# Kernel optimization log

Measured on AMD Instinct MI355X. Metric: run time of the kernel, lower is better.

The kernel has to match this reference:

```python
import jax, jax.numpy as jnp
import numpy as np

N, E, D, K = 50000, 600000, 128, 8
EPS = 1e-09


def setup_inputs() -> dict:
    key = jax.random.key(0)
    ks = jax.random.split(key, 10)
    feature = jax.random.normal(ks[0], (N, D), dtype=jnp.float32)
    snorm_n = jax.random.uniform(ks[1], (N, 1), dtype=jnp.float32)
    src = jax.random.randint(ks[2], (E,), 0, N, dtype=jnp.int32)
    dst = jax.random.randint(ks[3], (E,), 0, N, dtype=jnp.int32)
    W_low = jax.random.normal(ks[4], (D, D), dtype=jnp.float32) / np.sqrt(D)
    W_high = jax.random.normal(ks[5], (D, D), dtype=jnp.float32) / np.sqrt(D)
    W_mid = jax.random.normal(ks[6], (D, D), dtype=jnp.float32) / np.sqrt(D)
    gamma_low = jax.random.uniform(ks[7], (K,), dtype=jnp.float32)
    gamma_high = jax.random.uniform(ks[8], (K,), dtype=jnp.float32)
    gamma_mid = jax.random.uniform(ks[9], (K,), dtype=jnp.float32)
    bias = jnp.zeros((D,), dtype=jnp.float32)
    return {"feature": feature, "snorm_n": snorm_n, "src": src, "dst": dst,
            "W_low": W_low, "W_high": W_high, "W_mid": W_mid,
            "gamma_low": gamma_low, "gamma_high": gamma_high,
            "gamma_mid": gamma_mid, "bias": bias}


def _mp(feat, src, dst, norm):
    # symmetric-normalized SpMM: h[v] = norm[v] * sum_{u->v} norm[u]*feat[u]
    msg = (feat * norm[:, None])[src]                        # [E, D] gather
    agg = jax.ops.segment_sum(msg, dst, num_segments=N)       # [N, D] scatter-add
    return agg * norm[:, None]


def reference(feature, snorm_n, src, dst, W_low, W_high, W_mid,
              gamma_low, gamma_high, gamma_mid, bias):
    deg = jax.ops.segment_sum(jnp.ones((E,), feature.dtype), dst, num_segments=N)
    norm = jnp.clip(deg, 1.0) ** -0.5                          # in-degree^-0.5
    alpha = jnp.linspace(EPS, 1.0 - EPS, K).astype(feature.dtype)
    midalpha = jnp.linspace(EPS, 1.0, K).astype(feature.dtype)

    h = _mp(feature, src, dst, norm)

    gl = jax.nn.relu(gamma_low)
    o0 = (jnp.dot(alpha, gl) * h + jnp.dot(1.0 - alpha, gl) * feature) @ W_low.T
    gh = jax.nn.relu(gamma_high)
    o1 = (jnp.dot(-alpha, gh) * h + jnp.dot(1.0 - alpha, gh) * feature) @ W_high.T
    gm = jax.nn.relu(gamma_mid)
    h1 = _mp(h, src, dst, norm)
    o2 = (jnp.sum(gm) * h1 - jnp.dot(midalpha, gm) * feature) @ W_mid.T

    # sequential mutual gating, exactly as the torch in-place updates
    o0 = o0 * jax.nn.sigmoid(o1 + o2)
    o1 = o1 * jax.nn.sigmoid(o0 + o2)
    o2 = o2 * jax.nn.sigmoid(o0 + o1)

    out = o0 + o1 + o2 + bias
    out = out * snorm_n          # graph_norm
    out = jax.nn.relu(out)       # activation
    return out
```

## Files before the change

### kernel.cpp

```cpp
#include <hip/hip_runtime.h>
#include <hip/hip_bf16.h>
#include <math.h>

#define N_NODES 50000
#define N_EDGES 600000
#define DIM 128
#define KGAM 8
#define EPSV 1e-9f

#define CHUNK_SHIFT 11
#define NCHUNKS 25

typedef __attribute__((ext_vector_type(8))) short short8;
typedef __attribute__((ext_vector_type(4))) float float4v;

__device__ __forceinline__ float bf2f(short s) {
    unsigned int u = ((unsigned int)(unsigned short)s) << 16;
    return __builtin_bit_cast(float, u);
}
__device__ __forceinline__ short f2bf(float f) {
    return (short)__builtin_bit_cast(unsigned short, __float2bfloat16(f));
}
__device__ __forceinline__ unsigned int pack2(float a, float b) {
    return (unsigned int)(unsigned short)f2bf(a) | ((unsigned int)(unsigned short)f2bf(b) << 16);
}
__device__ __forceinline__ float sigm(float x) { return 1.f / (1.f + __expf(-x)); }
__device__ __forceinline__ float ulo(unsigned int u) { return __builtin_bit_cast(float, u << 16); }
__device__ __forceinline__ float uhi(unsigned int u) { return __builtin_bit_cast(float, u & 0xffff0000u); }

__global__ void k_prep_deg(const float4* __restrict__ feat4,
                           const float* __restrict__ W0, const float* __restrict__ W1,
                           const float* __restrict__ W2,
                           const float* __restrict__ gl, const float* __restrict__ gh,
                           const float* __restrict__ gm,
                           const int* __restrict__ dst,
                           uint4* __restrict__ fb4, unsigned int* __restrict__ Wb,
                           float* __restrict__ coeffs, int* __restrict__ deg) {
    int b = blockIdx.x, tid = threadIdx.x;
    if (b < 3125) {
        int idx = b * 256 + tid;
        float4 v0 = feat4[idx * 2];
        float4 v1 = feat4[idx * 2 + 1];
        uint4 o;
        o.x = pack2(v0.x, v0.y); o.y = pack2(v0.z, v0.w);
        o.z = pack2(v1.x, v1.y); o.w = pack2(v1.z, v1.w);
        fb4[idx] = o;
    } else if (b < 3173) {
        int j = (b - 3125) * 256 + tid;
        int g = j >> 12;
        int i = (j & 4095) * 4;
        const float* Ws = (g == 0) ? W0 : (g == 1) ? W1 : W2;
        float4 v = *(const float4*)(Ws + i);
        uint2 o; o.x = pack2(v.x, v.y); o.y = pack2(v.z, v.w);
        *(uint2*)(Wb + (g * DIM * DIM + i) / 2) = o;
    } else if (b == 3173) {
        if (tid == 0) {
            float a0 = 0, b0 = 0, a1 = 0, b1 = 0, sg = 0, m2 = 0;
            for (int k = 0; k < KGAM; ++k) {
                float al = EPSV + (float)k * (1.f - 2.f * EPSV) / (KGAM - 1);
                float md = EPSV + (float)k * (1.f - EPSV) / (KGAM - 1);
                float l = fmaxf(gl[k], 0.f), h = fmaxf(gh[k], 0.f), m = fmaxf(gm[k], 0.f);
                a0 += al * l;  b0 += (1.f - al) * l;
                a1 += -al * h; b1 += (1.f - al) * h;
                sg += m;       m2 += md * m;
            }
            coeffs[0] = a0; coeffs[1] = b0; coeffs[2] = a1;
            coeffs[3] = b1; coeffs[4] = sg; coeffs[5] = -m2;
        }
    } else {
        int e = (b - 3174) * 256 + tid;
        if (e < N_EDGES) atomicAdd(&deg[dst[e]], 1);
    }
}

__global__ __launch_bounds__(512) void k_scan(const int* __restrict__ deg,
                                              int* __restrict__ rowstart,
                                              int* __restrict__ bsums,
                                              float* __restrict__ norm,
                                              int* __restrict__ done) {
    __shared__ int s[512];
    __shared__ int lastf;
    __shared__ int bs[NCHUNKS];
    int tid = threadIdx.x;
    int i0 = blockIdx.x * 2048 + tid * 4;
    int v[4]; int sum = 0;
#pragma unroll
    for (int c = 0; c < 4; ++c) {
        int i = i0 + c;
        int d = (i < N_NODES) ? deg[i] : 0;
        v[c] = d; sum += d;
    }
    s[tid] = sum; __syncthreads();
#pragma unroll
    for (int off = 1; off < 512; off <<= 1) {
        int t = (tid >= off) ? s[tid - off] : 0;
        __syncthreads();
        s[tid] += t;
        __syncthreads();
    }
    if (tid == 511) bsums[blockIdx.x] = s[511];
    int run = s[tid] - sum;
#pragma unroll
    for (int c = 0; c < 4; ++c) {
        int i = i0 + c;
        if (i < N_NODES) {
            rowstart[i] = run;
            norm[i] = rsqrtf((float)(v[c] < 1 ? 1 : v[c]));
        }
        run += v[c];
    }
    __threadfence();
    __syncthreads();
    if (tid == 0) {
        int old = atomicAdd(done, 1);
        lastf = (old == (int)gridDim.x - 1) ? 1 : 0;
    }
    __syncthreads();
    if (lastf) {
        __threadfence();
        if (tid < NCHUNKS) bs[tid] = bsums[tid];
        __syncthreads();
        if (tid == 0) {
            int run2 = 0;
            for (int i = 0; i < NCHUNKS; ++i) { int t = bs[i]; bs[i] = run2; run2 += t; }
        }
        __syncthreads();
        if (tid < NCHUNKS) bsums[tid] = bs[tid];
    }
}

__global__ void k_fill(const int* __restrict__ src, const int* __restrict__ dst,
                       const int* __restrict__ rowstart, const int* __restrict__ bsums,
                       int* __restrict__ cnt, const float* __restrict__ norm,
                       uint2* __restrict__ er) {
    int e = blockIdx.x * blockDim.x + threadIdx.x;
    if (e < N_EDGES) {
        int d = dst[e];
        int slot = rowstart[d] + bsums[d >> CHUNK_SHIFT] + atomicAdd(&cnt[d], 1);
        int u = src[e];
        uint2 rec;
        rec.x = (unsigned int)u;
        rec.y = __builtin_bit_cast(unsigned int, norm[u]);
        er[slot] = rec;
    }
}

__device__ __forceinline__ void acc8(float4v& a0, float4v& a1, uint4 r, float nu) {
    a0.x = fmaf(nu, ulo(r.x), a0.x); a0.y = fmaf(nu, uhi(r.x), a0.y);
    a0.z = fmaf(nu, ulo(r.y), a0.z); a0.w = fmaf(nu, uhi(r.y), a0.w);
    a1.x = fmaf(nu, ulo(r.z), a1.x); a1.y = fmaf(nu, uhi(r.z), a1.y);
    a1.z = fmaf(nu, ulo(r.w), a1.z); a1.w = fmaf(nu, uhi(r.w), a1.w);
}

__global__ __launch_bounds__(256, 6) void k_spmm(
    const uint4* __restrict__ in, const float* __restrict__ norm,
    const int* __restrict__ rowstart, const int* __restrict__ bsums,
    const uint2* __restrict__ er, uint4* __restrict__ out) {
    int node = blockIdx.x * 16 + (threadIdx.x >> 4);
    if (node >= N_NODES) return;
    int gl = threadIdx.x & 15;
    int beg = rowstart[node] + bsums[node >> CHUNK_SHIFT];
    int end = (node == N_NODES - 1)
                  ? N_EDGES
                  : rowstart[node + 1] + bsums[(node + 1) >> CHUNK_SHIFT];
    float4v a0 = {0.f, 0.f, 0.f, 0.f};
    float4v a1 = {0.f, 0.f, 0.f, 0.f};
    int t = beg;
    for (; t + 7 < end; t += 8) {
        uint2 e0 = er[t],     e1 = er[t + 1], e2 = er[t + 2], e3 = er[t + 3];
        uint2 e4 = er[t + 4], e5 = er[t + 5], e6 = er[t + 6], e7 = er[t + 7];
        uint4 r0 = in[e0.x * 16u + gl];
        uint4 r1 = in[e1.x * 16u + gl];
        uint4 r2 = in[e2.x * 16u + gl];
        uint4 r3 = in[e3.x * 16u + gl];
        uint4 r4 = in[e4.x * 16u + gl];
        uint4 r5 = in[e5.x * 16u + gl];
        uint4 r6 = in[e6.x * 16u + gl];
        uint4 r7 = in[e7.x * 16u + gl];
        acc8(a0, a1, r0, __builtin_bit_cast(float, e0.y));
        acc8(a0, a1, r1, __builtin_bit_cast(float, e1.y));
        acc8(a0, a1, r2, __builtin_bit_cast(float, e2.y));
        acc8(a0, a1, r3, __builtin_bit_cast(float, e3.y));
        acc8(a0, a1, r4, __builtin_bit_cast(float, e4.y));
        acc8(a0, a1, r5, __builtin_bit_cast(float, e5.y));
        acc8(a0, a1, r6, __builtin_bit_cast(float, e6.y));
        acc8(a0, a1, r7, __builtin_bit_cast(float, e7.y));
    }
    if (t + 3 < end) {
        uint2 e0 = er[t], e1 = er[t + 1], e2 = er[t + 2], e3 = er[t + 3];
        uint4 r0 = in[e0.x * 16u + gl];
        uint4 r1 = in[e1.x * 16u + gl];
        uint4 r2 = in[e2.x * 16u + gl];
        uint4 r3 = in[e3.x * 16u + gl];
        acc8(a0, a1, r0, __builtin_bit_cast(float, e0.y));
        acc8(a0, a1, r1, __builtin_bit_cast(float, e1.y));
        acc8(a0, a1, r2, __builtin_bit_cast(float, e2.y));
        acc8(a0, a1, r3, __builtin_bit_cast(float, e3.y));
        t += 4;
    }
    for (; t < end; ++t) {
        uint2 e = er[t];
        uint4 r = in[e.x * 16u + gl];
        acc8(a0, a1, r, __builtin_bit_cast(float, e.y));
    }
    float nv = norm[node];
    uint4 o;
    o.x = pack2(a0.x * nv, a0.y * nv); o.y = pack2(a0.z * nv, a0.w * nv);
    o.z = pack2(a1.x * nv, a1.y * nv); o.w = pack2(a1.z * nv, a1.w * nv);
    out[node * 16u + gl] = o;
}

#define RT 64
#define TSTR 136

__global__ __launch_bounds__(512, 4) void k_gemm_fused(
    const short* __restrict__ hB, const short* __restrict__ fB,
    const short* __restrict__ h1B, const short* __restrict__ Wb,
    const float* __restrict__ coeffs, const float* __restrict__ bias,
    const float* __restrict__ snorm, float* __restrict__ out) {
    __shared__ short Ts[3][RT * TSTR];

    const float c0 = coeffs[0], c1 = coeffs[1], c2 = coeffs[2];
    const float c3 = coeffs[3], c4 = coeffs[4], c5 = coeffs[5];
    const int r0 = blockIdx.x * RT;
    const int tid = threadIdx.x;

#pragma unroll
    for (int it = 0; it < 2; ++it) {
        int idx = tid + it * 512;
        int r = idx >> 4;
        int cg = (idx & 15) * 8;
        int row = r0 + r;
        short8 hv = {0,0,0,0,0,0,0,0}, fv = {0,0,0,0,0,0,0,0}, h1v = {0,0,0,0,0,0,0,0};
        if (row < N_NODES) {
            size_t base = (size_t)row * DIM + cg;
            hv  = *(const short8*)(hB + base);
            fv  = *(const short8*)(fB + base);
            h1v = *(const short8*)(h1B + base);
        }
        short8 t0, t1, t2;
#pragma unroll
        for (int j = 0; j < 8; ++j) {
            float hf = bf2f(hv[j]), ff = bf2f(fv[j]), h1f = bf2f(h1v[j]);
            t0[j] = f2bf(c0 * hf + c1 * ff);
            t1[j] = f2bf(c2 * hf + c3 * ff);
            t2[j] = f2bf(c4 * h1f + c5 * ff);
        }
        int la = r * TSTR + cg;
        *(short8*)&Ts[0][la] = t0;
        *(short8*)&Ts[1][la] = t1;
        *(short8*)&Ts[2][la] = t2;
    }
    __syncthreads();

    const int lane = tid & 63;
    const int ct = tid >> 6;
    const int m = lane & 15;
    const int quad = lane >> 4;

    float4v acc[3][4];
    const float4v zero = {0.f, 0.f, 0.f, 0.f};
#pragma unroll
    for (int g = 0; g < 3; ++g)
#pragma unroll
        for (int rt = 0; rt < 4; ++rt) acc[g][rt] = zero;

    const short* wbase = Wb + (ct * 16 + m) * DIM + quad * 8;
#pragma unroll
    for (int ks = 0; ks < 4; ++ks) {
        const short* wp = wbase + ks * 32;
        short8 b0 = *(const short8*)(wp);
        short8 b1 = *(const short8*)(wp + DIM * DIM);
        short8 b2 = *(const short8*)(wp + 2 * DIM * DIM);
#pragma unroll
        for (int rt = 0; rt < 4; ++rt) {
            int aoff = (rt * 16 + m) * TSTR + ks * 32 + quad * 8;
            short8 a0 = *(const short8*)&Ts[0][aoff];
            short8 a1 = *(const short8*)&Ts[1][aoff];
            short8 a2 = *(const short8*)&Ts[2][aoff];
            acc[0][rt] = __builtin_amdgcn_mfma_f32_16x16x32_bf16(a0, b0, acc[0][rt], 0, 0, 0);
            acc[1][rt] = __builtin_amdgcn_mfma_f32_16x16x32_bf16(a1, b1, acc[1][rt], 0, 0, 0);
            acc[2][rt] = __builtin_amdgcn_mfma_f32_16x16x32_bf16(a2, b2, acc[2][rt], 0, 0, 0);
        }
    }

    const int col = ct * 16 + m;
    const float bc = bias[col];
#pragma unroll
    for (int rt = 0; rt < 4; ++rt) {
#pragma unroll
        for (int r = 0; r < 4; ++r) {
            int row = r0 + rt * 16 + quad * 4 + r;
            if (row < N_NODES) {
                float sn = snorm[row];
                float o0 = acc[0][rt][r], o1 = acc[1][rt][r], o2 = acc[2][rt][r];
                float g0 = o0 * sigm(o1 + o2);
                float g1 = o1 * sigm(g0 + o2);
                float g2 = o2 * sigm(g0 + g1);
                float vv = (g0 + g1 + g2 + bc) * sn;
                out[(size_t)row * DIM + col] = fmaxf(vv, 0.f);
            }
        }
    }
}

extern "C" void kernel_launch(void* const* d_in, const int* in_sizes, int n_in,
                              void* d_out, int out_size, void* d_ws, size_t ws_size,
                              hipStream_t stream) {
    const float* feature = (const float*)d_in[0];
    const float* snorm   = (const float*)d_in[1];
    const int*   src     = (const int*)d_in[2];
    const int*   dst     = (const int*)d_in[3];
    const float* W_low   = (const float*)d_in[4];
    const float* W_high  = (const float*)d_in[5];
    const float* W_mid   = (const float*)d_in[6];
    const float* gl      = (const float*)d_in[7];
    const float* gh      = (const float*)d_in[8];
    const float* gm      = (const float*)d_in[9];
    const float* bias    = (const float*)d_in[10];
    float* out = (float*)d_out;

    char* w = (char*)d_ws;
    auto alloc = [&](size_t bytes) {
        char* p = w;
        w += (bytes + 255) & ~(size_t)255;
        return p;
    };
    int* deg      = (int*)alloc((size_t)N_NODES * 4);
    int* cnt      = (int*)alloc((size_t)N_NODES * 4);
    int* done     = (int*)alloc(256);
    size_t zero_bytes = (size_t)((char*)done - (char*)deg) + 256;
    float* norm   = (float*)alloc((size_t)N_NODES * 4);
    int* rowstart = (int*)alloc((size_t)(N_NODES + 1) * 4);
    int* bsums    = (int*)alloc(64 * 4);
    uint2* er     = (uint2*)alloc((size_t)N_EDGES * 8);
    float* coeffs = (float*)alloc(64 * 4);
    short* Wb     = (short*)alloc((size_t)3 * DIM * DIM * 2);
    short* fb     = (short*)alloc((size_t)N_NODES * DIM * 2);
    short* h      = (short*)alloc((size_t)N_NODES * DIM * 2);
    short* h1     = (short*)alloc((size_t)N_NODES * DIM * 2);

    hipMemsetAsync(deg, 0, zero_bytes, stream);
    k_prep_deg<<<3174 + 2344, 256, 0, stream>>>(
        (const float4*)feature, W_low, W_high, W_mid, gl, gh, gm, dst,
        (uint4*)fb, (unsigned int*)Wb, coeffs, deg);
    k_scan<<<NCHUNKS, 512, 0, stream>>>(deg, rowstart, bsums, norm, done);
    k_fill<<<(N_EDGES + 255) / 256, 256, 0, stream>>>(src, dst, rowstart, bsums,
                                                      cnt, norm, er);
    int spmm_blocks = (N_NODES + 15) / 16;
    k_spmm<<<spmm_blocks, 256, 0, stream>>>((const uint4*)fb, norm, rowstart, bsums,
                                            er, (uint4*)h);
    k_spmm<<<spmm_blocks, 256, 0, stream>>>((const uint4*)h, norm, rowstart, bsums,
                                            er, (uint4*)h1);
    k_gemm_fused<<<(N_NODES + RT - 1) / RT, 512, 0, stream>>>(
        h, fb, h1, Wb, coeffs, bias, snorm, out);
}
```

Measured before the change: 242.8 us.

## Fuse all stages into one persistent cooperative kernel with grid syncs

Replaces the six separate launches (prep/degree, scan, CSR fill, two SpMM passes, fused GEMM) with a single cooperative persistent kernel that steps through the phases using grid-wide syncs and grid-stride loops. The aim is to remove launch gaps and per-kernel tail effects. In exchange it adds six grid barriers, caps the grid at an occupancy-based size of at most 1024 blocks of 512 threads, and forces every phase onto the 512-thread, LDS-heavy GEMM configuration, which may reduce SpMM occupancy. The second cnt zeroing inside the kernel is redundant but harmless.

New measurement: 693.9 us. +185.8%, slower.

```diff
diff --git a/kernel.cpp b/kernel.cpp
--- a/kernel.cpp
+++ b/kernel.cpp
@@ -1,6 +1,9 @@
 #include <hip/hip_runtime.h>
+#include <hip/hip_cooperative_groups.h>
 #include <hip/hip_bf16.h>
 #include <math.h>
+
+namespace cg = cooperative_groups;
 
 #define N_NODES 50000
 #define N_EDGES 600000
@@ -11,6 +14,17 @@
 #define CHUNK_SHIFT 11
 #define NCHUNKS 25
 
+#define RT 64
+#define TSTR 136
+#define NTILES ((N_NODES + RT - 1) / RT)
+
+#define FB_ITEMS 800000
+#define WB_BASE  FB_ITEMS
+#define WB_ITEMS 12288
+#define CO_BASE  (WB_BASE + WB_ITEMS)
+#define DEG_BASE (CO_BASE + 1)
+#define P1_TOTAL (DEG_BASE + N_EDGES)
+
 typedef __attribute__((ext_vector_type(8))) short short8;
 typedef __attribute__((ext_vector_type(4))) float float4v;
 
@@ -27,123 +41,6 @@
 __device__ __forceinline__ float sigm(float x) { return 1.f / (1.f + __expf(-x)); }
 __device__ __forceinline__ float ulo(unsigned int u) { return __builtin_bit_cast(float, u << 16); }
 __device__ __forceinline__ float uhi(unsigned int u) { return __builtin_bit_cast(float, u & 0xffff0000u); }
-
-__global__ void k_prep_deg(const float4* __restrict__ feat4,
-                           const float* __restrict__ W0, const float* __restrict__ W1,
-                           const float* __restrict__ W2,
-                           const float* __restrict__ gl, const float* __restrict__ gh,
-                           const float* __restrict__ gm,
-                           const int* __restrict__ dst,
-                           uint4* __restrict__ fb4, unsigned int* __restrict__ Wb,
-                           float* __restrict__ coeffs, int* __restrict__ deg) {
-    int b = blockIdx.x, tid = threadIdx.x;
-    if (b < 3125) {
-        int idx = b * 256 + tid;
-        float4 v0 = feat4[idx * 2];
-        float4 v1 = feat4[idx * 2 + 1];
-        uint4 o;
-        o.x = pack2(v0.x, v0.y); o.y = pack2(v0.z, v0.w);
-        o.z = pack2(v1.x, v1.y); o.w = pack2(v1.z, v1.w);
-        fb4[idx] = o;
-    } else if (b < 3173) {
-        int j = (b - 3125) * 256 + tid;
-        int g = j >> 12;
-        int i = (j & 4095) * 4;
-        const float* Ws = (g == 0) ? W0 : (g == 1) ? W1 : W2;
-        float4 v = *(const float4*)(Ws + i);
-        uint2 o; o.x = pack2(v.x, v.y); o.y = pack2(v.z, v.w);
-        *(uint2*)(Wb + (g * DIM * DIM + i) / 2) = o;
-    } else if (b == 3173) {
-        if (tid == 0) {
-            float a0 = 0, b0 = 0, a1 = 0, b1 = 0, sg = 0, m2 = 0;
-            for (int k = 0; k < KGAM; ++k) {
-                float al = EPSV + (float)k * (1.f - 2.f * EPSV) / (KGAM - 1);
-                float md = EPSV + (float)k * (1.f - EPSV) / (KGAM - 1);
-                float l = fmaxf(gl[k], 0.f), h = fmaxf(gh[k], 0.f), m = fmaxf(gm[k], 0.f);
-                a0 += al * l;  b0 += (1.f - al) * l;
-                a1 += -al * h; b1 += (1.f - al) * h;
-                sg += m;       m2 += md * m;
-            }
-            coeffs[0] = a0; coeffs[1] = b0; coeffs[2] = a1;
-            coeffs[3] = b1; coeffs[4] = sg; coeffs[5] = -m2;
-        }
-    } else {
-        int e = (b - 3174) * 256 + tid;
-        if (e < N_EDGES) atomicAdd(&deg[dst[e]], 1);
-    }
-}
-
-__global__ __launch_bounds__(512) void k_scan(const int* __restrict__ deg,
-                                              int* __restrict__ rowstart,
-                                              int* __restrict__ bsums,
-                                              float* __restrict__ norm,
-                                              int* __restrict__ done) {
-    __shared__ int s[512];
-    __shared__ int lastf;
-    __shared__ int bs[NCHUNKS];
-    int tid = threadIdx.x;
-    int i0 = blockIdx.x * 2048 + tid * 4;
-    int v[4]; int sum = 0;
-#pragma unroll
-    for (int c = 0; c < 4; ++c) {
-        int i = i0 + c;
-        int d = (i < N_NODES) ? deg[i] : 0;
-        v[c] = d; sum += d;
-    }
-    s[tid] = sum; __syncthreads();
-#pragma unroll
-    for (int off = 1; off < 512; off <<= 1) {
-        int t = (tid >= off) ? s[tid - off] : 0;
-        __syncthreads();
-        s[tid] += t;
-        __syncthreads();
-    }
-    if (tid == 511) bsums[blockIdx.x] = s[511];
-    int run = s[tid] - sum;
-#pragma unroll
-    for (int c = 0; c < 4; ++c) {
-        int i = i0 + c;
-        if (i < N_NODES) {
-            rowstart[i] = run;
-            norm[i] = rsqrtf((float)(v[c] < 1 ? 1 : v[c]));
-        }
-        run += v[c];
-    }
-    __threadfence();
-    __syncthreads();
-    if (tid == 0) {
-        int old = atomicAdd(done, 1);
-        lastf = (old == (int)gridDim.x - 1) ? 1 : 0;
-    }
-    __syncthreads();
-    if (lastf) {
-        __threadfence();
-        if (tid < NCHUNKS) bs[tid] = bsums[tid];
-        __syncthreads();
-        if (tid == 0) {
-            int run2 = 0;
-            for (int i = 0; i < NCHUNKS; ++i) { int t = bs[i]; bs[i] = run2; run2 += t; }
-        }
-        __syncthreads();
-        if (tid < NCHUNKS) bsums[tid] = bs[tid];
-    }
-}
-
-__global__ void k_fill(const int* __restrict__ src, const int* __restrict__ dst,
-                       const int* __restrict__ rowstart, const int* __restrict__ bsums,
-                       int* __restrict__ cnt, const float* __restrict__ norm,
-                       uint2* __restrict__ er) {
-    int e = blockIdx.x * blockDim.x + threadIdx.x;
-    if (e < N_EDGES) {
-        int d = dst[e];
-        int slot = rowstart[d] + bsums[d >> CHUNK_SHIFT] + atomicAdd(&cnt[d], 1);
-        int u = src[e];
-        uint2 rec;
-        rec.x = (unsigned int)u;
-        rec.y = __builtin_bit_cast(unsigned int, norm[u]);
-        er[slot] = rec;
-    }
-}
 
 __device__ __forceinline__ void acc8(float4v& a0, float4v& a1, uint4 r, float nu) {
     a0.x = fmaf(nu, ulo(r.x), a0.x); a0.y = fmaf(nu, uhi(r.x), a0.y);
@@ -152,153 +49,292 @@
     a1.z = fmaf(nu, ulo(r.w), a1.z); a1.w = fmaf(nu, uhi(r.w), a1.w);
 }
 
-__global__ __launch_bounds__(256, 6) void k_spmm(
-    const uint4* __restrict__ in, const float* __restrict__ norm,
-    const int* __restrict__ rowstart, const int* __restrict__ bsums,
-    const uint2* __restrict__ er, uint4* __restrict__ out) {
-    int node = blockIdx.x * 16 + (threadIdx.x >> 4);
-    if (node >= N_NODES) return;
-    int gl = threadIdx.x & 15;
-    int beg = rowstart[node] + bsums[node >> CHUNK_SHIFT];
-    int end = (node == N_NODES - 1)
-                  ? N_EDGES
-                  : rowstart[node + 1] + bsums[(node + 1) >> CHUNK_SHIFT];
-    float4v a0 = {0.f, 0.f, 0.f, 0.f};
-    float4v a1 = {0.f, 0.f, 0.f, 0.f};
-    int t = beg;
-    for (; t + 7 < end; t += 8) {
-        uint2 e0 = er[t],     e1 = er[t + 1], e2 = er[t + 2], e3 = er[t + 3];
-        uint2 e4 = er[t + 4], e5 = er[t + 5], e6 = er[t + 6], e7 = er[t + 7];
-        uint4 r0 = in[e0.x * 16u + gl];
-        uint4 r1 = in[e1.x * 16u + gl];
-        uint4 r2 = in[e2.x * 16u + gl];
-        uint4 r3 = in[e3.x * 16u + gl];
-        uint4 r4 = in[e4.x * 16u + gl];
-        uint4 r5 = in[e5.x * 16u + gl];
-        uint4 r6 = in[e6.x * 16u + gl];
-        uint4 r7 = in[e7.x * 16u + gl];
-        acc8(a0, a1, r0, __builtin_bit_cast(float, e0.y));
-        acc8(a0, a1, r1, __builtin_bit_cast(float, e1.y));
-        acc8(a0, a1, r2, __builtin_bit_cast(float, e2.y));
-        acc8(a0, a1, r3, __builtin_bit_cast(float, e3.y));
-        acc8(a0, a1, r4, __builtin_bit_cast(float, e4.y));
-        acc8(a0, a1, r5, __builtin_bit_cast(float, e5.y));
-        acc8(a0, a1, r6, __builtin_bit_cast(float, e6.y));
-        acc8(a0, a1, r7, __builtin_bit_cast(float, e7.y));
-    }
-    if (t + 3 < end) {
-        uint2 e0 = er[t], e1 = er[t + 1], e2 = er[t + 2], e3 = er[t + 3];
-        uint4 r0 = in[e0.x * 16u + gl];
-        uint4 r1 = in[e1.x * 16u + gl];
-        uint4 r2 = in[e2.x * 16u + gl];
-        uint4 r3 = in[e3.x * 16u + gl];
-        acc8(a0, a1, r0, __builtin_bit_cast(float, e0.y));
-        acc8(a0, a1, r1, __builtin_bit_cast(float, e1.y));
-        acc8(a0, a1, r2, __builtin_bit_cast(float, e2.y));
-        acc8(a0, a1, r3, __builtin_bit_cast(float, e3.y));
-        t += 4;
-    }
-    for (; t < end; ++t) {
-        uint2 e = er[t];
-        uint4 r = in[e.x * 16u + gl];
-        acc8(a0, a1, r, __builtin_bit_cast(float, e.y));
-    }
-    float nv = norm[node];
-    uint4 o;
-    o.x = pack2(a0.x * nv, a0.y * nv); o.y = pack2(a0.z * nv, a0.w * nv);
-    o.z = pack2(a1.x * nv, a1.y * nv); o.w = pack2(a1.z * nv, a1.w * nv);
-    out[node * 16u + gl] = o;
-}
-
-#define RT 64
-#define TSTR 136
-
-__global__ __launch_bounds__(512, 4) void k_gemm_fused(
-    const short* __restrict__ hB, const short* __restrict__ fB,
-    const short* __restrict__ h1B, const short* __restrict__ Wb,
-    const float* __restrict__ coeffs, const float* __restrict__ bias,
-    const float* __restrict__ snorm, float* __restrict__ out) {
+struct MegaArgs {
+    const float4* __restrict__ feat4;
+    const float* __restrict__ W0;
+    const float* __restrict__ W1;
+    const float* __restrict__ W2;
+    const float* __restrict__ gl;
+    const float* __restrict__ gh;
+    const float* __restrict__ gm;
+    const int* __restrict__ src;
+    const int* __restrict__ dst;
+    const float* __restrict__ snorm;
+    const float* __restrict__ bias;
+    uint4* __restrict__ fb4;
+    unsigned int* __restrict__ Wb;
+    float* __restrict__ coeffs;
+    int* __restrict__ deg;
+    int* __restrict__ cnt;
+    int* __restrict__ rowstart;
+    int* __restrict__ bsums;
+    float* __restrict__ norm;
+    uint2* __restrict__ er;
+    uint4* __restrict__ h4;
+    uint4* __restrict__ h14;
+    float* __restrict__ out;
+};
+
+__device__ __forceinline__ void spmm_phase(const uint4* __restrict__ in,
+                                           uint4* __restrict__ out,
+                                           const int* __restrict__ rowstart,
+                                           const int* __restrict__ bsums,
+                                           const float* __restrict__ norm,
+                                           const uint2* __restrict__ er,
+                                           int bid, int tid, int G) {
+    for (int base = bid * 32; base < N_NODES; base += G * 32) {
+        int node = base + (tid >> 4);
+        if (node >= N_NODES) continue;
+        int gl = tid & 15;
+        int beg = rowstart[node] + bsums[node >> CHUNK_SHIFT];
+        int end = (node == N_NODES - 1)
+                      ? N_EDGES
+                      : rowstart[node + 1] + bsums[(node + 1) >> CHUNK_SHIFT];
+        float4v a0 = {0.f, 0.f, 0.f, 0.f};
+        float4v a1 = {0.f, 0.f, 0.f, 0.f};
+        int t = beg;
+        for (; t + 7 < end; t += 8) {
+            uint2 e0 = er[t],     e1 = er[t + 1], e2 = er[t + 2], e3 = er[t + 3];
+            uint2 e4 = er[t + 4], e5 = er[t + 5], e6 = er[t + 6], e7 = er[t + 7];
+            uint4 r0 = in[e0.x * 16u + gl];
+            uint4 r1 = in[e1.x * 16u + gl];
+            uint4 r2 = in[e2.x * 16u + gl];
+            uint4 r3 = in[e3.x * 16u + gl];
+            uint4 r4 = in[e4.x * 16u + gl];
+            uint4 r5 = in[e5.x * 16u + gl];
+            uint4 r6 = in[e6.x * 16u + gl];
+            uint4 r7 = in[e7.x * 16u + gl];
+            acc8(a0, a1, r0, __builtin_bit_cast(float, e0.y));
+            acc8(a0, a1, r1, __builtin_bit_cast(float, e1.y));
+            acc8(a0, a1, r2, __builtin_bit_cast(float, e2.y));
+            acc8(a0, a1, r3, __builtin_bit_cast(float, e3.y));
+            acc8(a0, a1, r4, __builtin_bit_cast(float, e4.y));
+            acc8(a0, a1, r5, __builtin_bit_cast(float, e5.y));
+            acc8(a0, a1, r6, __builtin_bit_cast(float, e6.y));
+            acc8(a0, a1, r7, __builtin_bit_cast(float, e7.y));
+        }
+        if (t + 3 < end) {
+            uint2 e0 = er[t], e1 = er[t + 1], e2 = er[t + 2], e3 = er[t + 3];
+            uint4 r0 = in[e0.x * 16u + gl];
+            uint4 r1 = in[e1.x * 16u + gl];
+            uint4 r2 = in[e2.x * 16u + gl];
+            uint4 r3 = in[e3.x * 16u + gl];
+            acc8(a0, a1, r0, __builtin_bit_cast(float, e0.y));
+            acc8(a0, a1, r1, __builtin_bit_cast(float, e1.y));
+            acc8(a0, a1, r2, __builtin_bit_cast(float, e2.y));
+            acc8(a0, a1, r3, __builtin_bit_cast(float, e3.y));
+            t += 4;
+        }
+        for (; t < end; ++t) {
+            uint2 e = er[t];
+            uint4 r = in[e.x * 16u + gl];
+            acc8(a0, a1, r, __builtin_bit_cast(float, e.y));
+        }
+        float nv = norm[node];
+        uint4 o;
+        o.x = pack2(a0.x * nv, a0.y * nv); o.y = pack2(a0.z * nv, a0.w * nv);
+        o.z = pack2(a1.x * nv, a1.y * nv); o.w = pack2(a1.z * nv, a1.w * nv);
+        out[node * 16u + gl] = o;
+    }
+}
+
+__global__ __launch_bounds__(512, 4) void k_mega(MegaArgs a) {
+    cg::grid_group grid = cg::this_grid();
     __shared__ short Ts[3][RT * TSTR];
-
-    const float c0 = coeffs[0], c1 = coeffs[1], c2 = coeffs[2];
-    const float c3 = coeffs[3], c4 = coeffs[4], c5 = coeffs[5];
-    const int r0 = blockIdx.x * RT;
     const int tid = threadIdx.x;
-
-#pragma unroll
-    for (int it = 0; it < 2; ++it) {
-        int idx = tid + it * 512;
-        int r = idx >> 4;
-        int cg = (idx & 15) * 8;
-        int row = r0 + r;
-        short8 hv = {0,0,0,0,0,0,0,0}, fv = {0,0,0,0,0,0,0,0}, h1v = {0,0,0,0,0,0,0,0};
-        if (row < N_NODES) {
-            size_t base = (size_t)row * DIM + cg;
-            hv  = *(const short8*)(hB + base);
-            fv  = *(const short8*)(fB + base);
-            h1v = *(const short8*)(h1B + base);
-        }
-        short8 t0, t1, t2;
-#pragma unroll
-        for (int j = 0; j < 8; ++j) {
-            float hf = bf2f(hv[j]), ff = bf2f(fv[j]), h1f = bf2f(h1v[j]);
-            t0[j] = f2bf(c0 * hf + c1 * ff);
-            t1[j] = f2bf(c2 * hf + c3 * ff);
-            t2[j] = f2bf(c4 * h1f + c5 * ff);
-        }
-        int la = r * TSTR + cg;
-        *(short8*)&Ts[0][la] = t0;
-        *(short8*)&Ts[1][la] = t1;
-        *(short8*)&Ts[2][la] = t2;
-    }
-    __syncthreads();
+    const int bid = blockIdx.x;
+    const int G = gridDim.x;
+    const int gs = G * 512;
+
+    for (int i = bid * 512 + tid; i < P1_TOTAL; i += gs) {
+        if (i < FB_ITEMS) {
+            float4 v0 = a.feat4[(size_t)i * 2];
+            float4 v1 = a.feat4[(size_t)i * 2 + 1];
+            uint4 o;
+            o.x = pack2(v0.x, v0.y); o.y = pack2(v0.z, v0.w);
+            o.z = pack2(v1.x, v1.y); o.w = pack2(v1.z, v1.w);
+            a.fb4[i] = o;
+        } else if (i < CO_BASE) {
+            int j = i - WB_BASE;
+            int g = j >> 12;
+            int i4 = (j & 4095) * 4;
+            const float* Ws = (g == 0) ? a.W0 : (g == 1) ? a.W1 : a.W2;
+            float4 v = *(const float4*)(Ws + i4);
+            uint2 o; o.x = pack2(v.x, v.y); o.y = pack2(v.z, v.w);
+            *(uint2*)(a.Wb + (g * DIM * DIM + i4) / 2) = o;
+        } else if (i == CO_BASE) {
+            float a0 = 0, b0 = 0, a1 = 0, b1 = 0, sg = 0, m2 = 0;
+            for (int k = 0; k < KGAM; ++k) {
+                float al = EPSV + (float)k * (1.f - 2.f * EPSV) / (KGAM - 1);
+                float md = EPSV + (float)k * (1.f - EPSV) / (KGAM - 1);
+                float l = fmaxf(a.gl[k], 0.f), h = fmaxf(a.gh[k], 0.f), m = fmaxf(a.gm[k], 0.f);
+                a0 += al * l;  b0 += (1.f - al) * l;
+                a1 += -al * h; b1 += (1.f - al) * h;
+                sg += m;       m2 += md * m;
+            }
+            a.coeffs[0] = a0; a.coeffs[1] = b0; a.coeffs[2] = a1;
+            a.coeffs[3] = b1; a.coeffs[4] = sg; a.coeffs[5] = -m2;
+        } else {
+            int e = i - DEG_BASE;
+            atomicAdd(&a.deg[a.dst[e]], 1);
+        }
+    }
+    __threadfence();
+    grid.sync();
+
+    for (int i = bid * 512 + tid; i < N_NODES; i += gs) a.cnt[i] = 0;
+    if (bid < NCHUNKS) {
+        int* s = (int*)&Ts[0][0];
+        int i0 = bid * 2048 + tid * 4;
+        int v[4]; int sum = 0;
+#pragma unroll
+        for (int c = 0; c < 4; ++c) {
+            int i = i0 + c;
+            int d = (i < N_NODES) ? a.deg[i] : 0;
+            v[c] = d; sum += d;
+        }
+        s[tid] = sum; __syncthreads();
+#pragma unroll
+        for (int off = 1; off < 512; off <<= 1) {
+            int t = (tid >= off) ? s[tid - off] : 0;
+            __syncthreads();
+            s[tid] += t;
+            __syncthreads();
+        }
+        if (tid == 511) a.bsums[bid] = s[511];
+        int run = s[tid] - sum;
+#pragma unroll
+        for (int c = 0; c < 4; ++c) {
+            int i = i0 + c;
+            if (i < N_NODES) {
+                a.rowstart[i] = run;
+                a.norm[i] = rsqrtf((float)(v[c] < 1 ? 1 : v[c]));
+            }
+            run += v[c];
+        }
+    }
+    __threadfence();
+    grid.sync();
+
+    if (bid == 0) {
+        int* s = (int*)&Ts[0][0];
+        if (tid < NCHUNKS) s[tid] = a.bsums[tid];
+        __syncthreads();
+        if (tid == 0) {
+            int run = 0;
+            for (int i = 0; i < NCHUNKS; ++i) { int t = s[i]; s[i] = run; run += t; }
+        }
+        __syncthreads();
+        if (tid < NCHUNKS) a.bsums[tid] = s[tid];
+        __threadfence();
+    }
+    grid.sync();
+
+    for (int e = bid * 512 + tid; e < N_EDGES; e += gs) {
+        int d = a.dst[e];
+        int slot = a.rowstart[d] + a.bsums[d >> CHUNK_SHIFT] + atomicAdd(&a.cnt[d], 1);
+        int u = a.src[e];
+        uint2 rec;
+        rec.x = (unsigned int)u;
+        rec.y = __builtin_bit_cast(unsigned int, a.norm[u]);
+        a.er[slot] = rec;
+    }
+    __threadfence();
+    grid.sync();
+
+    spmm_phase(a.fb4, a.h4, a.rowstart, a.bsums, a.norm, a.er, bid, tid, G);
+    __threadfence();
+    grid.sync();
+
+    spmm_phase(a.h4, a.h14, a.rowstart, a.bsums, a.norm, a.er, bid, tid, G);
+    __threadfence();
+    grid.sync();
+
+    const short* hB  = (const short*)a.h4;
+    const short* fB  = (const short*)a.fb4;
+    const short* h1B = (const short*)a.h14;
+    const short* Wbs = (const short*)a.Wb;
+    const float c0 = a.coeffs[0], c1 = a.coeffs[1], c2 = a.coeffs[2];
+    const float c3 = a.coeffs[3], c4 = a.coeffs[4], c5 = a.coeffs[5];
 
     const int lane = tid & 63;
     const int ct = tid >> 6;
     const int m = lane & 15;
     const int quad = lane >> 4;
 
-    float4v acc[3][4];
-    const float4v zero = {0.f, 0.f, 0.f, 0.f};
-#pragma unroll
-    for (int g = 0; g < 3; ++g)
-#pragma unroll
-        for (int rt = 0; rt < 4; ++rt) acc[g][rt] = zero;
-
-    const short* wbase = Wb + (ct * 16 + m) * DIM + quad * 8;
-#pragma unroll
-    for (int ks = 0; ks < 4; ++ks) {
-        const short* wp = wbase + ks * 32;
-        short8 b0 = *(const short8*)(wp);
-        short8 b1 = *(const short8*)(wp + DIM * DIM);
-        short8 b2 = *(const short8*)(wp + 2 * DIM * DIM);
+    for (int tile = bid; tile < NTILES; tile += G) {
+        const int r0 = tile * RT;
+        __syncthreads();
+#pragma unroll
+        for (int it = 0; it < 2; ++it) {
+            int idx = tid + it * 512;
+            int r = idx >> 4;
+            int cg = (idx & 15) * 8;
+            int row = r0 + r;
+            short8 hv = {0,0,0,0,0,0,0,0}, fv = {0,0,0,0,0,0,0,0}, h1v = {0,0,0,0,0,0,0,0};
+            if (row < N_NODES) {
+                size_t base = (size_t)row * DIM + cg;
+                hv  = *(const short8*)(hB + base);
+                fv  = *(const short8*)(fB + base);
+                h1v = *(const short8*)(h1B + base);
+            }
+            short8 t0, t1, t2;
+#pragma unroll
+            for (int j = 0; j < 8; ++j) {
+                float hf = bf2f(hv[j]), ff = bf2f(fv[j]), h1f = bf2f(h1v[j]);
+                t0[j] = f2bf(c0 * hf + c1 * ff);
+                t1[j] = f2bf(c2 * hf + c3 * ff);
+                t2[j] = f2bf(c4 * h1f + c5 * ff);
+            }
+            int la = r * TSTR + cg;
+            *(short8*)&Ts[0][la] = t0;
+            *(short8*)&Ts[1][la] = t1;
+            *(short8*)&Ts[2][la] = t2;
+        }
+        __syncthreads();
+
+        float4v acc[3][4];
+        const float4v zero = {0.f, 0.f, 0.f, 0.f};
+#pragma unroll
+        for (int g = 0; g < 3; ++g)
+#pragma unroll
+            for (int rt = 0; rt < 4; ++rt) acc[g][rt] = zero;
+
+        const short* wbase = Wbs + (ct * 16 + m) * DIM + quad * 8;
+#pragma unroll
+        for (int ks = 0; ks < 4; ++ks) {
+            const short* wp = wbase + ks * 32;
+            short8 b0 = *(const short8*)(wp);
+            short8 b1 = *(const short8*)(wp + DIM * DIM);
+            short8 b2 = *(const short8*)(wp + 2 * DIM * DIM);
+#pragma unroll
+            for (int rt = 0; rt < 4; ++rt) {
+                int aoff = (rt * 16 + m) * TSTR + ks * 32 + quad * 8;
+                short8 a0 = *(const short8*)&Ts[0][aoff];
+                short8 a1 = *(const short8*)&Ts[1][aoff];
+                short8 a2 = *(const short8*)&Ts[2][aoff];
+                acc[0][rt] = __builtin_amdgcn_mfma_f32_16x16x32_bf16(a0, b0, acc[0][rt], 0, 0, 0);
+                acc[1][rt] = __builtin_amdgcn_mfma_f32_16x16x32_bf16(a1, b1, acc[1][rt], 0, 0, 0);
+                acc[2][rt] = __builtin_amdgcn_mfma_f32_16x16x32_bf16(a2, b2, acc[2][rt], 0, 0, 0);
+            }
+        }
+
+        const int col = ct * 16 + m;
+        const float bc = a.bias[col];
 #pragma unroll
         for (int rt = 0; rt < 4; ++rt) {
-            int aoff = (rt * 16 + m) * TSTR + ks * 32 + quad * 8;
-            short8 a0 = *(const short8*)&Ts[0][aoff];
-            short8 a1 = *(const short8*)&Ts[1][aoff];
-            short8 a2 = *(const short8*)&Ts[2][aoff];
-            acc[0][rt] = __builtin_amdgcn_mfma_f32_16x16x32_bf16(a0, b0, acc[0][rt], 0, 0, 0);
-            acc[1][rt] = __builtin_amdgcn_mfma_f32_16x16x32_bf16(a1, b1, acc[1][rt], 0, 0, 0);
-            acc[2][rt] = __builtin_amdgcn_mfma_f32_16x16x32_bf16(a2, b2, acc[2][rt], 0, 0, 0);
-        }
-    }
-
-    const int col = ct * 16 + m;
-    const float bc = bias[col];
-#pragma unroll
-    for (int rt = 0; rt < 4; ++rt) {
-#pragma unroll
-        for (int r = 0; r < 4; ++r) {
-            int row = r0 + rt * 16 + quad * 4 + r;
-            if (row < N_NODES) {
-                float sn = snorm[row];
-                float o0 = acc[0][rt][r], o1 = acc[1][rt][r], o2 = acc[2][rt][r];
-                float g0 = o0 * sigm(o1 + o2);
-                float g1 = o1 * sigm(g0 + o2);
-                float g2 = o2 * sigm(g0 + g1);
-                float vv = (g0 + g1 + g2 + bc) * sn;
-                out[(size_t)row * DIM + col] = fmaxf(vv, 0.f);
+#pragma unroll
+            for (int r = 0; r < 4; ++r) {
+                int row = r0 + rt * 16 + quad * 4 + r;
+                if (row < N_NODES) {
+                    float sn = a.snorm[row];
+                    float o0 = acc[0][rt][r], o1 = acc[1][rt][r], o2 = acc[2][rt][r];
+                    float g0 = o0 * sigm(o1 + o2);
+                    float g1 = o1 * sigm(g0 + o2);
+                    float g2 = o2 * sigm(g0 + g1);
+                    float vv = (g0 + g1 + g2 + bc) * sn;
+                    a.out[(size_t)row * DIM + col] = fmaxf(vv, 0.f);
+                }
             }
         }
     }
@@ -328,8 +364,7 @@
     };
     int* deg      = (int*)alloc((size_t)N_NODES * 4);
     int* cnt      = (int*)alloc((size_t)N_NODES * 4);
-    int* done     = (int*)alloc(256);
-    size_t zero_bytes = (size_t)((char*)done - (char*)deg) + 256;
+    size_t zero_bytes = (size_t)((char*)cnt - (char*)deg) + (size_t)N_NODES * 4;
     float* norm   = (float*)alloc((size_t)N_NODES * 4);
     int* rowstart = (int*)alloc((size_t)(N_NODES + 1) * 4);
     int* bsums    = (int*)alloc(64 * 4);
@@ -341,17 +376,26 @@
     short* h1     = (short*)alloc((size_t)N_NODES * DIM * 2);
 
     hipMemsetAsync(deg, 0, zero_bytes, stream);
-    k_prep_deg<<<3174 + 2344, 256, 0, stream>>>(
-        (const float4*)feature, W_low, W_high, W_mid, gl, gh, gm, dst,
-        (uint4*)fb, (unsigned int*)Wb, coeffs, deg);
-    k_scan<<<NCHUNKS, 512, 0, stream>>>(deg, rowstart, bsums, norm, done);
-    k_fill<<<(N_EDGES + 255) / 256, 256, 0, stream>>>(src, dst, rowstart, bsums,
-                                                      cnt, norm, er);
-    int spmm_blocks = (N_NODES + 15) / 16;
-    k_spmm<<<spmm_blocks, 256, 0, stream>>>((const uint4*)fb, norm, rowstart, bsums,
-                                            er, (uint4*)h);
-    k_spmm<<<spmm_blocks, 256, 0, stream>>>((const uint4*)h, norm, rowstart, bsums,
-                                            er, (uint4*)h1);
-    k_gemm_fused<<<(N_NODES + RT - 1) / RT, 512, 0, stream>>>(
-        h, fb, h1, Wb, coeffs, bias, snorm, out);
-}
+
+    int nb = 0;
+    hipError_t oerr = hipOccupancyMaxActiveBlocksPerMultiprocessor(&nb, k_mega, 512, 0);
+    if (oerr != hipSuccess || nb < 1) nb = 1;
+    int grid = nb * 256;
+    if (grid > 1024) grid = 1024;
+
+    MegaArgs margs;
+    margs.feat4 = (const float4*)feature;
+    margs.W0 = W_low; margs.W1 = W_high; margs.W2 = W_mid;
+    margs.gl = gl; margs.gh = gh; margs.gm = gm;
+    margs.src = src; margs.dst = dst;
+    margs.snorm = snorm; margs.bias = bias;
+    margs.fb4 = (uint4*)fb; margs.Wb = (unsigned int*)Wb;
+    margs.coeffs = coeffs; margs.deg = deg; margs.cnt = cnt;
+    margs.rowstart = rowstart; margs.bsums = bsums; margs.norm = norm;
+    margs.er = er; margs.h4 = (uint4*)h; margs.h14 = (uint4*)h1;
+    margs.out = out;
+
+    void* params[] = { &margs };
+    hipLaunchCooperativeKernel((const void*)k_mega, dim3(grid), dim3(512),
+                               params, 0, stream);
+}
```

## Fuse second SpMM into fused GEMM kernel, computing h1 tile into LDS

Applied to the files above, without the earlier changes.

Removes the second k_spmm launch and the h1 workspace buffer. Each GEMM block now gathers neighbour rows of h for its 64 nodes and builds the h1 tile directly in shared memory before combining it with h and feature. This saves a kernel launch and the write and re-read of the h1 array, but the GEMM kernel now runs an irregular gather phase at lower per-thread unroll (4 instead of 8) and inside a 512-thread block that has fewer resident waves. Output stores also become nontemporal.

New measurement: 240.5 us. No clear change (-1.0%).

```diff
diff --git a/kernel.cpp b/kernel.cpp
--- a/kernel.cpp
+++ b/kernel.cpp
@@ -27,6 +27,13 @@
 __device__ __forceinline__ float sigm(float x) { return 1.f / (1.f + __expf(-x)); }
 __device__ __forceinline__ float ulo(unsigned int u) { return __builtin_bit_cast(float, u << 16); }
 __device__ __forceinline__ float uhi(unsigned int u) { return __builtin_bit_cast(float, u & 0xffff0000u); }
+
+__device__ __forceinline__ void acc8(float4v& a0, float4v& a1, uint4 r, float nu) {
+    a0.x = fmaf(nu, ulo(r.x), a0.x); a0.y = fmaf(nu, uhi(r.x), a0.y);
+    a0.z = fmaf(nu, ulo(r.y), a0.z); a0.w = fmaf(nu, uhi(r.y), a0.w);
+    a1.x = fmaf(nu, ulo(r.z), a1.x); a1.y = fmaf(nu, uhi(r.z), a1.y);
+    a1.z = fmaf(nu, ulo(r.w), a1.z); a1.w = fmaf(nu, uhi(r.w), a1.w);
+}
 
 __global__ void k_prep_deg(const float4* __restrict__ feat4,
                            const float* __restrict__ W0, const float* __restrict__ W1,
@@ -145,13 +152,6 @@
     }
 }
 
-__device__ __forceinline__ void acc8(float4v& a0, float4v& a1, uint4 r, float nu) {
-    a0.x = fmaf(nu, ulo(r.x), a0.x); a0.y = fmaf(nu, uhi(r.x), a0.y);
-    a0.z = fmaf(nu, ulo(r.y), a0.z); a0.w = fmaf(nu, uhi(r.y), a0.w);
-    a1.x = fmaf(nu, ulo(r.z), a1.x); a1.y = fmaf(nu, uhi(r.z), a1.y);
-    a1.z = fmaf(nu, ulo(r.w), a1.z); a1.w = fmaf(nu, uhi(r.w), a1.w);
-}
-
 __global__ __launch_bounds__(256, 6) void k_spmm(
     const uint4* __restrict__ in, const float* __restrict__ norm,
     const int* __restrict__ rowstart, const int* __restrict__ bsums,
@@ -214,8 +214,10 @@
 #define TSTR 136
 
 __global__ __launch_bounds__(512, 4) void k_gemm_fused(
-    const short* __restrict__ hB, const short* __restrict__ fB,
-    const short* __restrict__ h1B, const short* __restrict__ Wb,
+    const uint4* __restrict__ h4, const short* __restrict__ fB,
+    const short* __restrict__ Wb,
+    const int* __restrict__ rowstart, const int* __restrict__ bsums,
+    const float* __restrict__ norm, const uint2* __restrict__ er,
     const float* __restrict__ coeffs, const float* __restrict__ bias,
     const float* __restrict__ snorm, float* __restrict__ out) {
     __shared__ short Ts[3][RT * TSTR];
@@ -224,6 +226,48 @@
     const float c3 = coeffs[3], c4 = coeffs[4], c5 = coeffs[5];
     const int r0 = blockIdx.x * RT;
     const int tid = threadIdx.x;
+    const short* hB = (const short*)h4;
+
+    {
+        int grp = tid >> 4;
+        int gl  = tid & 15;
+#pragma unroll
+        for (int rr0 = 0; rr0 < RT; rr0 += 32) {
+            int rr = rr0 + grp;
+            int node = r0 + rr;
+            uint4 o = {0u, 0u, 0u, 0u};
+            if (node < N_NODES) {
+                int beg = rowstart[node] + bsums[node >> CHUNK_SHIFT];
+                int end = (node == N_NODES - 1)
+                              ? N_EDGES
+                              : rowstart[node + 1] + bsums[(node + 1) >> CHUNK_SHIFT];
+                float4v a0 = {0.f, 0.f, 0.f, 0.f};
+                float4v a1 = {0.f, 0.f, 0.f, 0.f};
+                int t = beg;
+                for (; t + 3 < end; t += 4) {
+                    uint2 e0 = er[t], e1 = er[t + 1], e2 = er[t + 2], e3 = er[t + 3];
+                    uint4 r0v = h4[e0.x * 16u + gl];
+                    uint4 r1v = h4[e1.x * 16u + gl];
+                    uint4 r2v = h4[e2.x * 16u + gl];
+                    uint4 r3v = h4[e3.x * 16u + gl];
+                    acc8(a0, a1, r0v, __builtin_bit_cast(float, e0.y));
+                    acc8(a0, a1, r1v, __builtin_bit_cast(float, e1.y));
+                    acc8(a0, a1, r2v, __builtin_bit_cast(float, e2.y));
+                    acc8(a0, a1, r3v, __builtin_bit_cast(float, e3.y));
+                }
+                for (; t < end; ++t) {
+                    uint2 e = er[t];
+                    uint4 r = h4[e.x * 16u + gl];
+                    acc8(a0, a1, r, __builtin_bit_cast(float, e.y));
+                }
+                float nv = norm[node];
+                o.x = pack2(a0.x * nv, a0.y * nv); o.y = pack2(a0.z * nv, a0.w * nv);
+                o.z = pack2(a1.x * nv, a1.y * nv); o.w = pack2(a1.z * nv, a1.w * nv);
+            }
+            *(uint4*)&Ts[2][rr * TSTR + gl * 8] = o;
+        }
+    }
+    __syncthreads();
 
 #pragma unroll
     for (int it = 0; it < 2; ++it) {
@@ -231,13 +275,14 @@
         int r = idx >> 4;
         int cg = (idx & 15) * 8;
         int row = r0 + r;
-        short8 hv = {0,0,0,0,0,0,0,0}, fv = {0,0,0,0,0,0,0,0}, h1v = {0,0,0,0,0,0,0,0};
+        int la = r * TSTR + cg;
+        short8 hv = {0,0,0,0,0,0,0,0}, fv = {0,0,0,0,0,0,0,0};
         if (row < N_NODES) {
             size_t base = (size_t)row * DIM + cg;
             hv  = *(const short8*)(hB + base);
             fv  = *(const short8*)(fB + base);
-            h1v = *(const short8*)(h1B + base);
-        }
+        }
+        short8 h1v = *(const short8*)&Ts[2][la];
         short8 t0, t1, t2;
 #pragma unroll
         for (int j = 0; j < 8; ++j) {
@@ -246,7 +291,6 @@
             t1[j] = f2bf(c2 * hf + c3 * ff);
             t2[j] = f2bf(c4 * h1f + c5 * ff);
         }
-        int la = r * TSTR + cg;
         *(short8*)&Ts[0][la] = t0;
         *(short8*)&Ts[1][la] = t1;
         *(short8*)&Ts[2][la] = t2;
@@ -298,7 +342,7 @@
                 float g1 = o1 * sigm(g0 + o2);
                 float g2 = o2 * sigm(g0 + g1);
                 float vv = (g0 + g1 + g2 + bc) * sn;
-                out[(size_t)row * DIM + col] = fmaxf(vv, 0.f);
+                __builtin_nontemporal_store(fmaxf(vv, 0.f), &out[(size_t)row * DIM + col]);
             }
         }
     }
@@ -338,7 +382,6 @@
     short* Wb     = (short*)alloc((size_t)3 * DIM * DIM * 2);
     short* fb     = (short*)alloc((size_t)N_NODES * DIM * 2);
     short* h      = (short*)alloc((size_t)N_NODES * DIM * 2);
-    short* h1     = (short*)alloc((size_t)N_NODES * DIM * 2);
 
     hipMemsetAsync(deg, 0, zero_bytes, stream);
     k_prep_deg<<<3174 + 2344, 256, 0, stream>>>(
@@ -347,11 +390,9 @@
     k_scan<<<NCHUNKS, 512, 0, stream>>>(deg, rowstart, bsums, norm, done);
     k_fill<<<(N_EDGES + 255) / 256, 256, 0, stream>>>(src, dst, rowstart, bsums,
                                                       cnt, norm, er);
-    int spmm_blocks = (N_NODES + 15) / 16;
-    k_spmm<<<spmm_blocks, 256, 0, stream>>>((const uint4*)fb, norm, rowstart, bsums,
-                                            er, (uint4*)h);
-    k_spmm<<<spmm_blocks, 256, 0, stream>>>((const uint4*)h, norm, rowstart, bsums,
-                                            er, (uint4*)h1);
+    k_spmm<<<(N_NODES + 15) / 16, 256, 0, stream>>>((const uint4*)fb, norm, rowstart,
+                                                    bsums, er, (uint4*)h);
     k_gemm_fused<<<(N_NODES + RT - 1) / RT, 512, 0, stream>>>(
-        h, fb, h1, Wb, coeffs, bias, snorm, out);
-}
+        (const uint4*)h, fb, Wb, rowstart, bsums, norm, er,
+        coeffs, bias, snorm, out);
+}
```

## Split SpMM into column-slice passes and halve GEMM row tile

Applied to the files above, without the earlier changes.

The SpMM kernel now splits the 128-wide feature dimension into four 32-column slices, each handled by a separate block range. Within a slice, a 16-lane group gathers 4-byte words instead of 16-byte vectors. The intent is to shrink the working set of gathered rows per pass so the scattered reads hit cache better. The cost is four reads of the edge list per SpMM and narrower, less efficient gather transactions. The fused GEMM row tile drops from 64 to 32 rows to launch more blocks, and the final output uses nontemporal stores.

Result: slower. 278.5 us (+14.7%).

```diff
diff --git a/kernel.cpp b/kernel.cpp
--- a/kernel.cpp
+++ b/kernel.cpp
@@ -10,6 +10,9 @@
 
 #define CHUNK_SHIFT 11
 #define NCHUNKS 25
+
+#define NPASS 4
+#define NBLK 3125
 
 typedef __attribute__((ext_vector_type(8))) short short8;
 typedef __attribute__((ext_vector_type(4))) float float4v;
@@ -145,72 +148,72 @@
     }
 }
 
-__device__ __forceinline__ void acc8(float4v& a0, float4v& a1, uint4 r, float nu) {
-    a0.x = fmaf(nu, ulo(r.x), a0.x); a0.y = fmaf(nu, uhi(r.x), a0.y);
-    a0.z = fmaf(nu, ulo(r.y), a0.z); a0.w = fmaf(nu, uhi(r.y), a0.w);
-    a1.x = fmaf(nu, ulo(r.z), a1.x); a1.y = fmaf(nu, uhi(r.z), a1.y);
-    a1.z = fmaf(nu, ulo(r.w), a1.z); a1.w = fmaf(nu, uhi(r.w), a1.w);
-}
-
-__global__ __launch_bounds__(256, 6) void k_spmm(
-    const uint4* __restrict__ in, const float* __restrict__ norm,
+__global__ __launch_bounds__(256, 6) void k_spmm_slice(
+    const unsigned int* __restrict__ in, const float* __restrict__ norm,
     const int* __restrict__ rowstart, const int* __restrict__ bsums,
-    const uint2* __restrict__ er, uint4* __restrict__ out) {
-    int node = blockIdx.x * 16 + (threadIdx.x >> 4);
-    if (node >= N_NODES) return;
-    int gl = threadIdx.x & 15;
+    const uint2* __restrict__ er, unsigned int* __restrict__ out) {
+    int bid = blockIdx.x;
+    int pass = bid / NBLK;
+    int nb = bid - pass * NBLK;
+    int grp = threadIdx.x >> 4;
+    int l = threadIdx.x & 15;
+    int node = nb * 16 + grp;
     int beg = rowstart[node] + bsums[node >> CHUNK_SHIFT];
     int end = (node == N_NODES - 1)
                   ? N_EDGES
                   : rowstart[node + 1] + bsums[(node + 1) >> CHUNK_SHIFT];
-    float4v a0 = {0.f, 0.f, 0.f, 0.f};
-    float4v a1 = {0.f, 0.f, 0.f, 0.f};
+    const unsigned int* ip = in + pass * 16 + l;
+    float ax = 0.f, ay = 0.f;
     int t = beg;
     for (; t + 7 < end; t += 8) {
         uint2 e0 = er[t],     e1 = er[t + 1], e2 = er[t + 2], e3 = er[t + 3];
         uint2 e4 = er[t + 4], e5 = er[t + 5], e6 = er[t + 6], e7 = er[t + 7];
-        uint4 r0 = in[e0.x * 16u + gl];
-        uint4 r1 = in[e1.x * 16u + gl];
-        uint4 r2 = in[e2.x * 16u + gl];
-        uint4 r3 = in[e3.x * 16u + gl];
-        uint4 r4 = in[e4.x * 16u + gl];
-        uint4 r5 = in[e5.x * 16u + gl];
-        uint4 r6 = in[e6.x * 16u + gl];
-        uint4 r7 = in[e7.x * 16u + gl];
-        acc8(a0, a1, r0, __builtin_bit_cast(float, e0.y));
-        acc8(a0, a1, r1, __builtin_bit_cast(float, e1.y));
-        acc8(a0, a1, r2, __builtin_bit_cast(float, e2.y));
-        acc8(a0, a1, r3, __builtin_bit_cast(float, e3.y));
-        acc8(a0, a1, r4, __builtin_bit_cast(float, e4.y));
-        acc8(a0, a1, r5, __builtin_bit_cast(float, e5.y));
-        acc8(a0, a1, r6, __builtin_bit_cast(float, e6.y));
-        acc8(a0, a1, r7, __builtin_bit_cast(float, e7.y));
+        unsigned int r0 = ip[e0.x * 64u];
+        unsigned int r1 = ip[e1.x * 64u];
+        unsigned int r2 = ip[e2.x * 64u];
+        unsigned int r3 = ip[e3.x * 64u];
+        unsigned int r4 = ip[e4.x * 64u];
+        unsigned int r5 = ip[e5.x * 64u];
+        unsigned int r6 = ip[e6.x * 64u];
+        unsigned int r7 = ip[e7.x * 64u];
+        float n0 = __builtin_bit_cast(float, e0.y), n1 = __builtin_bit_cast(float, e1.y);
+        float n2 = __builtin_bit_cast(float, e2.y), n3 = __builtin_bit_cast(float, e3.y);
+        float n4 = __builtin_bit_cast(float, e4.y), n5 = __builtin_bit_cast(float, e5.y);
+        float n6 = __builtin_bit_cast(float, e6.y), n7 = __builtin_bit_cast(float, e7.y);
+        ax = fmaf(n0, ulo(r0), ax); ay = fmaf(n0, uhi(r0), ay);
+        ax = fmaf(n1, ulo(r1), ax); ay = fmaf(n1, uhi(r1), ay);
+        ax = fmaf(n2, ulo(r2), ax); ay = fmaf(n2, uhi(r2), ay);
+        ax = fmaf(n3, ulo(r3), ax); ay = fmaf(n3, uhi(r3), ay);
+        ax = fmaf(n4, ulo(r4), ax); ay = fmaf(n4, uhi(r4), ay);
+        ax = fmaf(n5, ulo(r5), ax); ay = fmaf(n5, uhi(r5), ay);
+        ax = fmaf(n6, ulo(r6), ax); ay = fmaf(n6, uhi(r6), ay);
+        ax = fmaf(n7, ulo(r7), ax); ay = fmaf(n7, uhi(r7), ay);
     }
     if (t + 3 < end) {
         uint2 e0 = er[t], e1 = er[t + 1], e2 = er[t + 2], e3 = er[t + 3];
-        uint4 r0 = in[e0.x * 16u + gl];
-        uint4 r1 = in[e1.x * 16u + gl];
-        uint4 r2 = in[e2.x * 16u + gl];
-        uint4 r3 = in[e3.x * 16u + gl];
-        acc8(a0, a1, r0, __builtin_bit_cast(float, e0.y));
-        acc8(a0, a1, r1, __builtin_bit_cast(float, e1.y));
-        acc8(a0, a1, r2, __builtin_bit_cast(float, e2.y));
-        acc8(a0, a1, r3, __builtin_bit_cast(float, e3.y));
+        unsigned int r0 = ip[e0.x * 64u];
+        unsigned int r1 = ip[e1.x * 64u];
+        unsigned int r2 = ip[e2.x * 64u];
+        unsigned int r3 = ip[e3.x * 64u];
+        float n0 = __builtin_bit_cast(float, e0.y), n1 = __builtin_bit_cast(float, e1.y);
+        float n2 = __builtin_bit_cast(float, e2.y), n3 = __builtin_bit_cast(float, e3.y);
+        ax = fmaf(n0, ulo(r0), ax); ay = fmaf(n0, uhi(r0), ay);
+        ax = fmaf(n1, ulo(r1), ax); ay = fmaf(n1, uhi(r1), ay);
+        ax = fmaf(n2, ulo(r2), ax); ay = fmaf(n2, uhi(r2), ay);
+        ax = fmaf(n3, ulo(r3), ax); ay = fmaf(n3, uhi(r3), ay);
         t += 4;
     }
     for (; t < end; ++t) {
         uint2 e = er[t];
-        uint4 r = in[e.x * 16u + gl];
-        acc8(a0, a1, r, __builtin_bit_cast(float, e.y));
+        unsigned int r = ip[e.x * 64u];
+        float nu = __builtin_bit_cast(float, e.y);
+        ax = fmaf(nu, ulo(r), ax); ay = fmaf(nu, uhi(r), ay);
     }
     float nv = norm[node];
-    uint4 o;
-    o.x = pack2(a0.x * nv, a0.y * nv); o.y = pack2(a0.z * nv, a0.w * nv);
-    o.z = pack2(a1.x * nv, a1.y * nv); o.w = pack2(a1.z * nv, a1.w * nv);
-    out[node * 16u + gl] = o;
-}
-
-#define RT 64
+    out[(unsigned)node * 64u + pass * 16u + l] = pack2(ax * nv, ay * nv);
+}
+
+#define RT 32
 #define TSTR 136
 
 __global__ __launch_bounds__(512, 4) void k_gemm_fused(
@@ -225,12 +228,11 @@
     const int r0 = blockIdx.x * RT;
     const int tid = threadIdx.x;
 
-#pragma unroll
-    for (int it = 0; it < 2; ++it) {
-        int idx = tid + it * 512;
-        int r = idx >> 4;
-        int cg = (idx & 15) * 8;
+    {
+        int r = tid >> 4;
+        int cg = (tid & 15) * 8;
         int row = r0 + r;
+        int la = r * TSTR + cg;
         short8 hv = {0,0,0,0,0,0,0,0}, fv = {0,0,0,0,0,0,0,0}, h1v = {0,0,0,0,0,0,0,0};
         if (row < N_NODES) {
             size_t base = (size_t)row * DIM + cg;
@@ -246,7 +248,6 @@
             t1[j] = f2bf(c2 * hf + c3 * ff);
             t2[j] = f2bf(c4 * h1f + c5 * ff);
         }
-        int la = r * TSTR + cg;
         *(short8*)&Ts[0][la] = t0;
         *(short8*)&Ts[1][la] = t1;
         *(short8*)&Ts[2][la] = t2;
@@ -258,12 +259,12 @@
     const int m = lane & 15;
     const int quad = lane >> 4;
 
-    float4v acc[3][4];
+    float4v acc[3][2];
     const float4v zero = {0.f, 0.f, 0.f, 0.f};
 #pragma unroll
     for (int g = 0; g < 3; ++g)
 #pragma unroll
-        for (int rt = 0; rt < 4; ++rt) acc[g][rt] = zero;
+        for (int rt = 0; rt < 2; ++rt) acc[g][rt] = zero;
 
     const short* wbase = Wb + (ct * 16 + m) * DIM + quad * 8;
 #pragma unroll
@@ -273,7 +274,7 @@
         short8 b1 = *(const short8*)(wp + DIM * DIM);
         short8 b2 = *(const short8*)(wp + 2 * DIM * DIM);
 #pragma unroll
-        for (int rt = 0; rt < 4; ++rt) {
+        for (int rt = 0; rt < 2; ++rt) {
             int aoff = (rt * 16 + m) * TSTR + ks * 32 + quad * 8;
             short8 a0 = *(const short8*)&Ts[0][aoff];
             short8 a1 = *(const short8*)&Ts[1][aoff];
@@ -287,7 +288,7 @@
     const int col = ct * 16 + m;
     const float bc = bias[col];
 #pragma unroll
-    for (int rt = 0; rt < 4; ++rt) {
+    for (int rt = 0; rt < 2; ++rt) {
 #pragma unroll
         for (int r = 0; r < 4; ++r) {
             int row = r0 + rt * 16 + quad * 4 + r;
@@ -298,7 +299,7 @@
                 float g1 = o1 * sigm(g0 + o2);
                 float g2 = o2 * sigm(g0 + g1);
                 float vv = (g0 + g1 + g2 + bc) * sn;
-                out[(size_t)row * DIM + col] = fmaxf(vv, 0.f);
+                __builtin_nontemporal_store(fmaxf(vv, 0.f), &out[(size_t)row * DIM + col]);
             }
         }
     }
@@ -347,11 +348,10 @@
     k_scan<<<NCHUNKS, 512, 0, stream>>>(deg, rowstart, bsums, norm, done);
     k_fill<<<(N_EDGES + 255) / 256, 256, 0, stream>>>(src, dst, rowstart, bsums,
                                                       cnt, norm, er);
-    int spmm_blocks = (N_NODES + 15) / 16;
-    k_spmm<<<spmm_blocks, 256, 0, stream>>>((const uint4*)fb, norm, rowstart, bsums,
-                                            er, (uint4*)h);
-    k_spmm<<<spmm_blocks, 256, 0, stream>>>((const uint4*)h, norm, rowstart, bsums,
-                                            er, (uint4*)h1);
+    k_spmm_slice<<<NPASS * NBLK, 256, 0, stream>>>(
+        (const unsigned int*)fb, norm, rowstart, bsums, er, (unsigned int*)h);
+    k_spmm_slice<<<NPASS * NBLK, 256, 0, stream>>>(
+        (const unsigned int*)h, norm, rowstart, bsums, er, (unsigned int*)h1);
     k_gemm_fused<<<(N_NODES + RT - 1) / RT, 512, 0, stream>>>(
         h, fb, h1, Wb, coeffs, bias, snorm, out);
 }
```
